# Performance work log

Hardware: AMD Instinct MI355X
Metric: run time of the kernel (lower is better)

The kernel has to match this reference:

```python
import jax, jax.numpy as jnp
import numpy as np

N = 1024      # side of the square relation matrix
K = 64        # in_dim
OUT = 64      # out_dim
N_W = 15      # h_params_asym


def setup_inputs() -> dict:
    key = jax.random.key(0)
    k1, k2 = jax.random.split(key)
    S = N * N
    input_layer = jax.random.normal(k1, (S, K), dtype=jnp.float32)
    stdv = 1.0 / float(np.sqrt(K))
    weights = jax.random.uniform(k2, (N_W, K, OUT), minval=-stdv, maxval=stdv, dtype=jnp.float32)
    ar = jnp.arange(S, dtype=jnp.int32)
    rows = ar // N                       # row index of each flattened entry
    cols = ar % N                        # col index of each flattened entry
    idx_trans = cols * N + rows          # transpose permutation
    idx_diag = jnp.arange(N, dtype=jnp.int32) * (N + 1)  # diagonal positions
    idx_all = jnp.zeros((S,), dtype=jnp.int32)           # single segment
    idx_diag_broad = jnp.zeros((N,), dtype=jnp.int32)    # pool diag to one segment
    col_norm = jnp.full((N,), float(N), dtype=jnp.float32)   # each column-segment has N members
    row_norm = jnp.full((N,), float(N), dtype=jnp.float32)
    all_norm = jnp.array([float(S)], dtype=jnp.float32)
    diag_norm = jnp.array([float(N)], dtype=jnp.float32)
    return dict(input_layer=input_layer, weights=weights,
                idx_trans=idx_trans, idx_diag=idx_diag, idx_row=rows, idx_col=cols,
                idx_all=idx_all, idx_diag_broad=idx_diag_broad,
                col_norm=col_norm, row_norm=row_norm, all_norm=all_norm, diag_norm=diag_norm)


def reference(input_layer, weights, idx_trans, idx_diag, idx_row, idx_col,
              idx_all, idx_diag_broad, col_norm, row_norm, all_norm, diag_norm):
    S = input_layer.shape[0]
    n = idx_diag.shape[0]
    out_dim = weights.shape[2]

    def pool(X, idx, norm, nseg):
        # normalized segment mean (index_add then divide)
        return jax.ops.segment_sum(X, idx, num_segments=nseg) / norm[:, None]

    def scatter_diag(X):
        # scatter n rows onto the diagonal positions of an [S, out_dim] zero tensor
        return jnp.zeros((S, out_dim), X.dtype).at[idx_diag].set(X)

    transpose = input_layer[idx_trans]            # [S, k]
    diagonal = input_layer[idx_diag]              # [n, k]
    row_pool = pool(input_layer, idx_col, col_norm, n)   # [n, k]
    col_pool = pool(input_layer, idx_row, row_norm, n)   # [n, k]
    all_pool = pool(input_layer, idx_all, all_norm, 1)   # [1, k]
    diag_pool = pool(diagonal, idx_diag_broad, diag_norm, 1)  # [1, k]

    output = input_layer @ weights[0]
    output += transpose @ weights[1]
    output += scatter_diag(diagonal @ weights[2])
    output += (row_pool @ weights[3])[idx_col]    # row_pool broadcast over col idx
    output += (row_pool @ weights[4])[idx_row]    # row_pool broadcast over row idx
    output += (col_pool @ weights[5])[idx_row]
    output += (col_pool @ weights[6])[idx_col]
    output += (all_pool @ weights[7])[idx_all]
    output += scatter_diag((diag_pool @ weights[8])[idx_diag_broad])
    output += scatter_diag((all_pool @ weights[9])[idx_diag_broad])
    output += scatter_diag(row_pool @ weights[10])
    output += scatter_diag(col_pool @ weights[11])
    output += (diag_pool @ weights[12])[idx_all]
    output += (diagonal @ weights[13])[idx_col]
    output += (diagonal @ weights[14])[idx_row]
    return output
```

## Files before the change

kernel.cpp:

```cpp
#include <hip/hip_runtime.h>
#include <hip/hip_bf16.h>

typedef __attribute__((ext_vector_type(4))) short shortx4;
typedef __attribute__((ext_vector_type(8))) short short8;
typedef __attribute__((ext_vector_type(4))) float floatx4;

__device__ __forceinline__ unsigned short f2bf(float f) {
    __hip_bfloat16 h = __float2bfloat16(f);
    return __builtin_bit_cast(unsigned short, h);
}

#define GLOAD_LDS16(g, l) __builtin_amdgcn_global_load_lds(                      \
    (const __attribute__((address_space(1))) void*)(g),                          \
    (__attribute__((address_space(3))) void*)(l), 16, 0, 0)

__global__ __launch_bounds__(256) void sweep_kernel(const float* __restrict__ in,
        unsigned short* __restrict__ bfcopy, float* __restrict__ rowpart,
        float* __restrict__ colpart, float* __restrict__ diagbuf) {
    __shared__ float colp[4][16][64];
    int t = threadIdx.x;
    int kq = t & 15;
    int cl = (t >> 4) & 3;
    int w  = t >> 6;
    int c  = w * 4 + cl;
    int ti = blockIdx.y, tj = blockIdx.x;
    int R = ti * 16, C = tj * 16;
    const float* base = in + ((size_t)R << 16) + (size_t)(C + c) * 64 + kq * 4;
    unsigned short* tbase = bfcopy + ((size_t)(ti * 64 + tj) << 14);
    bool dt = (ti == tj);

    floatx4 rowacc = (floatx4){0.f, 0.f, 0.f, 0.f};
    #pragma unroll
    for (int i = 0; i < 16; ++i) {
        floatx4 v = __builtin_nontemporal_load((const floatx4*)(base + ((size_t)i << 16)));
        rowacc += v;
        int row = i * 16 + c;
        int wg = (kq >> 1) ^ ((row ^ (row >> 4)) & 7);
        shortx4 h;
        h[0] = (short)f2bf(v[0]); h[1] = (short)f2bf(v[1]);
        h[2] = (short)f2bf(v[2]); h[3] = (short)f2bf(v[3]);
        *(shortx4*)(tbase + (size_t)row * 64 + wg * 8 + (kq & 1) * 4) = h;
        if (dt && c == i)
            *(floatx4*)&diagbuf[(size_t)(R + i) * 64 + kq * 4] = v;
        floatx4 cs = v;
        #pragma unroll
        for (int m = 16; m <= 32; m <<= 1) {
            cs[0] += __shfl_xor(cs[0], m);
            cs[1] += __shfl_xor(cs[1], m);
            cs[2] += __shfl_xor(cs[2], m);
            cs[3] += __shfl_xor(cs[3], m);
        }
        if (cl == 0) *(floatx4*)&colp[w][i][kq * 4] = cs;
    }
    *(floatx4*)&rowpart[(size_t)ti * 65536 + (size_t)(C + c) * 64 + kq * 4] = rowacc;
    __syncthreads();
    int i2 = t >> 4, kq2 = t & 15;
    floatx4 s = *(const floatx4*)&colp[0][i2][kq2 * 4];
    s += *(const floatx4*)&colp[1][i2][kq2 * 4];
    s += *(const floatx4*)&colp[2][i2][kq2 * 4];
    s += *(const floatx4*)&colp[3][i2][kq2 * 4];
    *(floatx4*)&colpart[(size_t)tj * 65536 + (size_t)(R + i2) * 64 + kq2 * 4] = s;
}

__global__ __launch_bounds__(256) void finred_kernel(const float* __restrict__ rowpart,
        const float* __restrict__ diagbuf, const float* __restrict__ wts,
        float* __restrict__ allraw, float* __restrict__ diagraw,
        unsigned short* __restrict__ w0t, unsigned short* __restrict__ w1t) {
    __shared__ float red[4][64];
    int b = blockIdx.x, t = threadIdx.x;
    if (b < 64) {
        int o = t & 63, seg = t >> 6;
        float s = 0.f;
        #pragma unroll 4
        for (int y = 0; y < 64; ++y)
            #pragma unroll
            for (int cl = 0; cl < 4; ++cl) {
                int c = b * 16 + seg * 4 + cl;
                s += rowpart[(size_t)y * 65536 + (size_t)c * 64 + o];
            }
        red[seg][o] = s;
        __syncthreads();
        if (t < 64)
            atomicAdd(&allraw[t], red[0][t] + red[1][t] + red[2][t] + red[3][t]);
    } else if (b < 72) {
        int d = b - 64;
        int k = t & 63, rl = t >> 6;
        float sd = 0.f;
        #pragma unroll 8
        for (int u = 0; u < 32; ++u)
            sd += diagbuf[(size_t)(d * 128 + rl + 4 * u) * 64 + k];
        red[rl][k] = sd;
        __syncthreads();
        if (t < 64)
            atomicAdd(&diagraw[t], red[0][t] + red[1][t] + red[2][t] + red[3][t]);
    } else {
        int idx = (b - 72) * 256 + t;
        int n = idx >> 6, k = idx & 63;
        w0t[idx] = f2bf(wts[k * 64 + n]);
        w1t[idx] = f2bf(wts[4096 + k * 64 + n]);
    }
}

__global__ __launch_bounds__(256) void abd_kernel(const float* __restrict__ W,
        const float* __restrict__ rowpart, const float* __restrict__ colpart,
        const float* __restrict__ diagbuf, const float* __restrict__ allraw,
        const float* __restrict__ diagraw,
        float* __restrict__ Ab, float* __restrict__ Bb, float* __restrict__ Dgb) {
    __shared__ float rp[4][64], cp[4][64], dv[4][64], ap[64], dp[64];
    int t = threadIdx.x, o = t & 63, il = t >> 6;
    int i0 = blockIdx.x * 4;
    int i = i0 + il;
    float sr = 0.f;
    #pragma unroll 8
    for (int y = 0; y < 64; ++y)
        sr += rowpart[(size_t)y * 65536 + (size_t)i * 64 + o];
    rp[il][o] = sr * (1.f / 1024.f);
    float sc = 0.f;
    #pragma unroll 8
    for (int y = 0; y < 64; ++y)
        sc += colpart[(size_t)y * 65536 + (size_t)i * 64 + o];
    cp[il][o] = sc * (1.f / 1024.f);
    dv[il][o] = diagbuf[i * 64 + o];
    if (t < 64) {
        ap[t] = allraw[t] * (1.f / 1048576.f);
        dp[t] = diagraw[t] * (1.f / 1024.f);
    }
    __syncthreads();
    float aA = 0.f, aB = 0.f, aD = 0.f, cA = 0.f, cD = 0.f;
    #pragma unroll 4
    for (int k = 0; k < 64; ++k) {
        int ko = k * 64 + o;
        float rA = rp[il][k], cAk = cp[il][k], dA = dv[il][k];
        aA += rA * W[3 * 4096 + ko] + cAk * W[6 * 4096 + ko] + dA * W[13 * 4096 + ko];
        aB += rA * W[4 * 4096 + ko] + cAk * W[5 * 4096 + ko] + dA * W[14 * 4096 + ko];
        aD += dA * W[2 * 4096 + ko] + rA * W[10 * 4096 + ko] + cAk * W[11 * 4096 + ko];
        cA += ap[k] * W[7 * 4096 + ko] + dp[k] * W[12 * 4096 + ko];
        cD += dp[k] * W[8 * 4096 + ko] + ap[k] * W[9 * 4096 + ko];
    }
    Ab[i * 64 + o]  = aA + cA;
    Bb[i * 64 + o]  = aB;
    Dgb[i * 64 + o] = aD + cD;
}

__global__ __launch_bounds__(256, 2) void main_kernel(const unsigned short* __restrict__ bfcopy,
        const unsigned short* __restrict__ w0t, const unsigned short* __restrict__ w1t,
        const float* __restrict__ Ab, const float* __restrict__ Bb,
        const float* __restrict__ Dgb, float* __restrict__ out) {
    __shared__ short lds[32768];

    int t = threadIdx.x;
    int lane = t & 63, w = t >> 6;
    int lrow = lane & 15, lhi = lane >> 4;

    int p = blockIdx.x;
    float fb = (129.0f - sqrtf(129.0f * 129.0f - 8.0f * (float)p)) * 0.5f;
    int bi = (int)fb;
    while (bi > 0 && bi * (129 - bi) / 2 > p) --bi;
    while ((bi + 1) * (129 - (bi + 1)) / 2 <= p) ++bi;
    int bj = bi + (p - bi * (129 - bi) / 2);
    int r0 = bi * 16, c0 = bj * 16;
    bool diag = (bi == bj);

    const unsigned short* t0 = bfcopy + ((size_t)(bi * 64 + bj) << 14);
    const unsigned short* t1 = bfcopy + ((size_t)(bj * 64 + bi) << 14);
    #pragma unroll
    for (int n = 0; n < 8; ++n) {
        int g = n * 256 + t;
        GLOAD_LDS16(t0 + g * 8, lds + g * 8);
    }
    if (!diag) {
        #pragma unroll
        for (int n = 0; n < 8; ++n) {
            int g = n * 256 + t;
            GLOAD_LDS16(t1 + g * 8, lds + 16384 + g * 8);
        }
    }

    short8 bw0[2][4], bw1[2][4];
    #pragma unroll
    for (int kg = 0; kg < 2; ++kg)
        #pragma unroll
        for (int nt = 0; nt < 4; ++nt) {
            int off = (nt * 16 + lrow) * 64 + kg * 32 + lhi * 8;
            bw0[kg][nt] = *(const short8*)(w0t + off);
            bw1[kg][nt] = *(const short8*)(w1t + off);
        }
    float pA[2][4][4], pB[2][4][4];
    #pragma unroll
    for (int sel = 0; sel < 2; ++sel) {
        int rbase = sel ? c0 : r0;
        int cbase = sel ? r0 : c0;
        #pragma unroll
        for (int x = 0; x < 4; ++x)
            #pragma unroll
            for (int nt = 0; nt < 4; ++nt) {
                pA[sel][x][nt] = Ab[(cbase + lhi * 4 + x) * 64 + nt * 16 + lrow];
                pB[sel][x][nt] = Bb[(rbase + w * 4 + x) * 64 + nt * 16 + lrow];
            }
    }
    __syncthreads();

    int base1 = diag ? 0 : 16384;

    #pragma unroll
    for (int sel = 0; sel < 2; ++sel) {
        if (sel == 1 && diag) continue;
        int selb = sel ? base1 : 0;
        int othb = sel ? 0 : base1;
        int rbase = sel ? c0 : r0;
        int cbase = sel ? r0 : c0;
        #pragma unroll
        for (int mf = 0; mf < 4; ++mf) {
            int I = w * 4 + mf;
            int mrow = I * 16 + lrow;
            int swzm = (mrow ^ (mrow >> 4)) & 7;
            int trow = lrow * 16 + I;
            int swzt = (trow ^ (trow >> 4)) & 7;
            short8 ad[2], at2[2];
            #pragma unroll
            for (int kg = 0; kg < 2; ++kg) {
                ad[kg]  = *(const short8*)(lds + selb + mrow * 64 + ((kg * 4 + lhi) ^ swzm) * 8);
                at2[kg] = *(const short8*)(lds + othb + trow * 64 + ((kg * 4 + lhi) ^ swzt) * 8);
            }
            floatx4 acc[4];
            #pragma unroll
            for (int nt = 0; nt < 4; ++nt) acc[nt] = (floatx4){0.f, 0.f, 0.f, 0.f};
            #pragma unroll
            for (int nt = 0; nt < 4; ++nt) {
                acc[nt] = __builtin_amdgcn_mfma_f32_16x16x32_bf16(ad[0],  bw0[0][nt], acc[nt], 0, 0, 0);
                acc[nt] = __builtin_amdgcn_mfma_f32_16x16x32_bf16(ad[1],  bw0[1][nt], acc[nt], 0, 0, 0);
                acc[nt] = __builtin_amdgcn_mfma_f32_16x16x32_bf16(at2[0], bw1[0][nt], acc[nt], 0, 0, 0);
                acc[nt] = __builtin_amdgcn_mfma_f32_16x16x32_bf16(at2[1], bw1[1][nt], acc[nt], 0, 0, 0);
            }
            int ridx = rbase + I;
            #pragma unroll
            for (int jj = 0; jj < 4; ++jj) {
                int j = lhi * 4 + jj;
                int cidx = cbase + j;
                size_t s = ((size_t)ridx << 10) + cidx;
                bool isd = diag && (I == j);
                #pragma unroll
                for (int nt = 0; nt < 4; ++nt) {
                    float v = acc[nt][jj] + pA[sel][jj][nt] + pB[sel][mf][nt];
                    if (isd) v += Dgb[ridx * 64 + nt * 16 + lrow];
                    __builtin_nontemporal_store(v, &out[s * 64 + nt * 16 + lrow]);
                }
            }
        }
    }
}

extern "C" void kernel_launch(void* const* d_in, const int* in_sizes, int n_in,
                              void* d_out, int out_size, void* d_ws, size_t ws_size,
                              hipStream_t stream) {
    const float* in  = (const float*)d_in[0];
    const float* wts = (const float*)d_in[1];
    float* out = (float*)d_out;
    float* ws = (float*)d_ws;

    unsigned short* bfcopy = (unsigned short*)ws;
    float* rowpart  = ws + 33554432;
    float* colpart  = ws + 37748736;
    float* diagbuf  = ws + 42074112;
    float* allraw   = ws + 42139648;
    float* diagraw  = ws + 42139712;
    float* Ab       = ws + 42139776;
    float* Bb       = ws + 42205312;
    float* Dgb      = ws + 42270848;
    unsigned short* w0t = (unsigned short*)(ws + 42336384);
    unsigned short* w1t = w0t + 4096;

    (void)hipMemsetAsync((void*)allraw, 0, 128 * sizeof(float), stream);

    sweep_kernel<<<dim3(64, 64), 256, 0, stream>>>(in, bfcopy, rowpart, colpart, diagbuf);
    finred_kernel<<<88, 256, 0, stream>>>(rowpart, diagbuf, wts, allraw, diagraw, w0t, w1t);
    abd_kernel<<<256, 256, 0, stream>>>(wts, rowpart, colpart, diagbuf,
                                        allraw, diagraw, Ab, Bb, Dgb);
    main_kernel<<<2080, 256, 0, stream>>>(bfcopy, w0t, w1t, Ab, Bb, Dgb, out);
}
```

Before: 207.5 us.

## Make main kernel persistent with double-buffered LDS prefetch of next tile pair

The main kernel becomes a persistent kernel: 256 blocks each loop over tile pairs with a stride of 256. While one pair is computed, the global-to-LDS load of the next pair goes into a second LDS buffer. The aim is to hide tile load latency and cut block launch overhead. In exchange, LDS doubles to 128 KB, occupancy drops to one block per CU, and only 256 blocks cover the grid. There is also a possible race, because the async LDS loads are not waited on explicitly before the next iteration reads them.

```diff
diff --git a/kernel.cpp b/kernel.cpp
--- a/kernel.cpp
+++ b/kernel.cpp
@@ -13,6 +13,15 @@
 #define GLOAD_LDS16(g, l) __builtin_amdgcn_global_load_lds(                      \
     (const __attribute__((address_space(1))) void*)(g),                          \
     (__attribute__((address_space(3))) void*)(l), 16, 0, 0)
+
+__device__ __forceinline__ void decode_pair(int p, int& bi, int& bj) {
+    float fb = (129.0f - sqrtf(129.0f * 129.0f - 8.0f * (float)p)) * 0.5f;
+    int b = (int)fb;
+    while (b > 0 && b * (129 - b) / 2 > p) --b;
+    while ((b + 1) * (129 - (b + 1)) / 2 <= p) ++b;
+    bi = b;
+    bj = b + (p - b * (129 - b) / 2);
+}
 
 __global__ __launch_bounds__(256) void sweep_kernel(const float* __restrict__ in,
         unsigned short* __restrict__ bfcopy, float* __restrict__ rowpart,
@@ -142,39 +151,15 @@
     Dgb[i * 64 + o] = aD + cD;
 }
 
-__global__ __launch_bounds__(256, 2) void main_kernel(const unsigned short* __restrict__ bfcopy,
+__global__ __launch_bounds__(256, 1) void main_kernel(const unsigned short* __restrict__ bfcopy,
         const unsigned short* __restrict__ w0t, const unsigned short* __restrict__ w1t,
         const float* __restrict__ Ab, const float* __restrict__ Bb,
         const float* __restrict__ Dgb, float* __restrict__ out) {
-    __shared__ short lds[32768];
+    __shared__ short lds[65536];
 
     int t = threadIdx.x;
     int lane = t & 63, w = t >> 6;
     int lrow = lane & 15, lhi = lane >> 4;
-
-    int p = blockIdx.x;
-    float fb = (129.0f - sqrtf(129.0f * 129.0f - 8.0f * (float)p)) * 0.5f;
-    int bi = (int)fb;
-    while (bi > 0 && bi * (129 - bi) / 2 > p) --bi;
-    while ((bi + 1) * (129 - (bi + 1)) / 2 <= p) ++bi;
-    int bj = bi + (p - bi * (129 - bi) / 2);
-    int r0 = bi * 16, c0 = bj * 16;
-    bool diag = (bi == bj);
-
-    const unsigned short* t0 = bfcopy + ((size_t)(bi * 64 + bj) << 14);
-    const unsigned short* t1 = bfcopy + ((size_t)(bj * 64 + bi) << 14);
-    #pragma unroll
-    for (int n = 0; n < 8; ++n) {
-        int g = n * 256 + t;
-        GLOAD_LDS16(t0 + g * 8, lds + g * 8);
-    }
-    if (!diag) {
-        #pragma unroll
-        for (int n = 0; n < 8; ++n) {
-            int g = n * 256 + t;
-            GLOAD_LDS16(t1 + g * 8, lds + 16384 + g * 8);
-        }
-    }
 
     short8 bw0[2][4], bw1[2][4];
     #pragma unroll
@@ -185,68 +170,119 @@
             bw0[kg][nt] = *(const short8*)(w0t + off);
             bw1[kg][nt] = *(const short8*)(w1t + off);
         }
-    float pA[2][4][4], pB[2][4][4];
-    #pragma unroll
-    for (int sel = 0; sel < 2; ++sel) {
-        int rbase = sel ? c0 : r0;
-        int cbase = sel ? r0 : c0;
-        #pragma unroll
-        for (int x = 0; x < 4; ++x)
-            #pragma unroll
-            for (int nt = 0; nt < 4; ++nt) {
-                pA[sel][x][nt] = Ab[(cbase + lhi * 4 + x) * 64 + nt * 16 + lrow];
-                pB[sel][x][nt] = Bb[(rbase + w * 4 + x) * 64 + nt * 16 + lrow];
-            }
+
+    int bi_c, bj_c;
+    decode_pair(blockIdx.x, bi_c, bj_c);
+    {
+        bool dg = (bi_c == bj_c);
+        const unsigned short* t0 = bfcopy + ((size_t)(bi_c * 64 + bj_c) << 14);
+        const unsigned short* t1 = bfcopy + ((size_t)(bj_c * 64 + bi_c) << 14);
+        #pragma unroll
+        for (int n = 0; n < 8; ++n) {
+            int g = n * 256 + t;
+            GLOAD_LDS16(t0 + g * 8, lds + g * 8);
+        }
+        if (!dg) {
+            #pragma unroll
+            for (int n = 0; n < 8; ++n) {
+                int g = n * 256 + t;
+                GLOAD_LDS16(t1 + g * 8, lds + 16384 + g * 8);
+            }
+        }
     }
     __syncthreads();
 
-    int base1 = diag ? 0 : 16384;
-
-    #pragma unroll
-    for (int sel = 0; sel < 2; ++sel) {
-        if (sel == 1 && diag) continue;
-        int selb = sel ? base1 : 0;
-        int othb = sel ? 0 : base1;
-        int rbase = sel ? c0 : r0;
-        int cbase = sel ? r0 : c0;
-        #pragma unroll
-        for (int mf = 0; mf < 4; ++mf) {
-            int I = w * 4 + mf;
-            int mrow = I * 16 + lrow;
-            int swzm = (mrow ^ (mrow >> 4)) & 7;
-            int trow = lrow * 16 + I;
-            int swzt = (trow ^ (trow >> 4)) & 7;
-            short8 ad[2], at2[2];
-            #pragma unroll
-            for (int kg = 0; kg < 2; ++kg) {
-                ad[kg]  = *(const short8*)(lds + selb + mrow * 64 + ((kg * 4 + lhi) ^ swzm) * 8);
-                at2[kg] = *(const short8*)(lds + othb + trow * 64 + ((kg * 4 + lhi) ^ swzt) * 8);
-            }
-            floatx4 acc[4];
-            #pragma unroll
-            for (int nt = 0; nt < 4; ++nt) acc[nt] = (floatx4){0.f, 0.f, 0.f, 0.f};
-            #pragma unroll
-            for (int nt = 0; nt < 4; ++nt) {
-                acc[nt] = __builtin_amdgcn_mfma_f32_16x16x32_bf16(ad[0],  bw0[0][nt], acc[nt], 0, 0, 0);
-                acc[nt] = __builtin_amdgcn_mfma_f32_16x16x32_bf16(ad[1],  bw0[1][nt], acc[nt], 0, 0, 0);
-                acc[nt] = __builtin_amdgcn_mfma_f32_16x16x32_bf16(at2[0], bw1[0][nt], acc[nt], 0, 0, 0);
-                acc[nt] = __builtin_amdgcn_mfma_f32_16x16x32_bf16(at2[1], bw1[1][nt], acc[nt], 0, 0, 0);
-            }
-            int ridx = rbase + I;
-            #pragma unroll
-            for (int jj = 0; jj < 4; ++jj) {
-                int j = lhi * 4 + jj;
-                int cidx = cbase + j;
-                size_t s = ((size_t)ridx << 10) + cidx;
-                bool isd = diag && (I == j);
+    int cur = 0;
+    for (int p = blockIdx.x; p < 2080; p += 256) {
+        int pn = p + 256;
+        int bi_n = 0, bj_n = 0;
+        if (pn < 2080) {
+            decode_pair(pn, bi_n, bj_n);
+            int nb = (cur ^ 1) * 32768;
+            bool dg = (bi_n == bj_n);
+            const unsigned short* t0 = bfcopy + ((size_t)(bi_n * 64 + bj_n) << 14);
+            const unsigned short* t1 = bfcopy + ((size_t)(bj_n * 64 + bi_n) << 14);
+            #pragma unroll
+            for (int n = 0; n < 8; ++n) {
+                int g = n * 256 + t;
+                GLOAD_LDS16(t0 + g * 8, lds + nb + g * 8);
+            }
+            if (!dg) {
+                #pragma unroll
+                for (int n = 0; n < 8; ++n) {
+                    int g = n * 256 + t;
+                    GLOAD_LDS16(t1 + g * 8, lds + nb + 16384 + g * 8);
+                }
+            }
+        }
+
+        int r0 = bi_c * 16, c0 = bj_c * 16;
+        bool diag = (bi_c == bj_c);
+        int cb = cur * 32768;
+
+        float pA[2][4][4], pB[2][4][4];
+        #pragma unroll
+        for (int sel = 0; sel < 2; ++sel) {
+            int rbase = sel ? c0 : r0;
+            int cbase = sel ? r0 : c0;
+            #pragma unroll
+            for (int x = 0; x < 4; ++x)
                 #pragma unroll
                 for (int nt = 0; nt < 4; ++nt) {
-                    float v = acc[nt][jj] + pA[sel][jj][nt] + pB[sel][mf][nt];
-                    if (isd) v += Dgb[ridx * 64 + nt * 16 + lrow];
-                    __builtin_nontemporal_store(v, &out[s * 64 + nt * 16 + lrow]);
-                }
-            }
-        }
+                    pA[sel][x][nt] = Ab[(cbase + lhi * 4 + x) * 64 + nt * 16 + lrow];
+                    pB[sel][x][nt] = Bb[(rbase + w * 4 + x) * 64 + nt * 16 + lrow];
+                }
+        }
+
+        int base1 = diag ? cb : cb + 16384;
+        #pragma unroll
+        for (int sel = 0; sel < 2; ++sel) {
+            if (sel == 1 && diag) continue;
+            int selb = sel ? base1 : cb;
+            int othb = sel ? cb : base1;
+            int rbase = sel ? c0 : r0;
+            int cbase = sel ? r0 : c0;
+            #pragma unroll
+            for (int mf = 0; mf < 4; ++mf) {
+                int I = w * 4 + mf;
+                int mrow = I * 16 + lrow;
+                int swzm = (mrow ^ (mrow >> 4)) & 7;
+                int trow = lrow * 16 + I;
+                int swzt = (trow ^ (trow >> 4)) & 7;
+                short8 ad[2], at2[2];
+                #pragma unroll
+                for (int kg = 0; kg < 2; ++kg) {
+                    ad[kg]  = *(const short8*)(lds + selb + mrow * 64 + ((kg * 4 + lhi) ^ swzm) * 8);
+                    at2[kg] = *(const short8*)(lds + othb + trow * 64 + ((kg * 4 + lhi) ^ swzt) * 8);
+                }
+                floatx4 acc[4];
+                #pragma unroll
+                for (int nt = 0; nt < 4; ++nt) acc[nt] = (floatx4){0.f, 0.f, 0.f, 0.f};
+                #pragma unroll
+                for (int nt = 0; nt < 4; ++nt) {
+                    acc[nt] = __builtin_amdgcn_mfma_f32_16x16x32_bf16(ad[0],  bw0[0][nt], acc[nt], 0, 0, 0);
+                    acc[nt] = __builtin_amdgcn_mfma_f32_16x16x32_bf16(ad[1],  bw0[1][nt], acc[nt], 0, 0, 0);
+                    acc[nt] = __builtin_amdgcn_mfma_f32_16x16x32_bf16(at2[0], bw1[0][nt], acc[nt], 0, 0, 0);
+                    acc[nt] = __builtin_amdgcn_mfma_f32_16x16x32_bf16(at2[1], bw1[1][nt], acc[nt], 0, 0, 0);
+                }
+                int ridx = rbase + I;
+                #pragma unroll
+                for (int jj = 0; jj < 4; ++jj) {
+                    int j = lhi * 4 + jj;
+                    int cidx = cbase + j;
+                    size_t s = ((size_t)ridx << 10) + cidx;
+                    bool isd = diag && (I == j);
+                    #pragma unroll
+                    for (int nt = 0; nt < 4; ++nt) {
+                        float v = acc[nt][jj] + pA[sel][jj][nt] + pB[sel][mf][nt];
+                        if (isd) v += Dgb[ridx * 64 + nt * 16 + lrow];
+                        __builtin_nontemporal_store(v, &out[s * 64 + nt * 16 + lrow]);
+                    }
+                }
+            }
+        }
+        __syncthreads();
+        bi_c = bi_n; bj_c = bj_n; cur ^= 1;
     }
 }
 
@@ -276,5 +312,5 @@
     finred_kernel<<<88, 256, 0, stream>>>(rowpart, diagbuf, wts, allraw, diagraw, w0t, w1t);
     abd_kernel<<<256, 256, 0, stream>>>(wts, rowpart, colpart, diagbuf,
                                         allraw, diagraw, Ab, Bb, Dgb);
-    main_kernel<<<2080, 256, 0, stream>>>(bfcopy, w0t, w1t, Ab, Bb, Dgb, out);
-}
+    main_kernel<<<256, 256, 0, stream>>>(bfcopy, w0t, w1t, Ab, Bb, Dgb, out);
+}
```

Result: slower. 212.7 us (+2.5%).
